# Kernel tuning notes

Hardware: AMD Instinct MI355X
Metric: run time of the kernel (lower is better)

The kernel has to match this reference:

```python
import jax, jax.numpy as jnp
import numpy as np

N, E = 50000, 800000
IN, HID, OUT, EH = 128, 64, 128, 32  # node dims, edge-MLP hidden=32
N_ETYPES, N_NTYPES = 3, 2


def setup_inputs() -> dict:
    key = jax.random.key(0)
    ks = jax.random.split(key, 12)
    w = lambda k, shape, fan: jax.random.normal(k, shape, jnp.float32) / np.float32(np.sqrt(fan))
    nf = jax.random.normal(ks[0], (N, IN), jnp.float32)
    edge_index = jax.random.randint(ks[1], (2, E), 0, N, dtype=jnp.int32)
    edge_type = jax.random.randint(ks[2], (E,), 0, N_ETYPES, dtype=jnp.int32)
    node_type = jax.random.randint(ks[3], (N,), 0, N_NTYPES, dtype=jnp.int32)
    return {
        "nf": nf,
        "edge_index": edge_index,
        "edge_type": edge_type,
        "node_type": node_type,
        # layer 0: 128 -> 64
        "eW0": w(ks[4], (N_ETYPES, 2 * IN, EH), 2 * IN),
        "eb0": jax.random.normal(ks[5], (N_ETYPES, EH), jnp.float32) * 0.01,
        "nW0": w(ks[6], (N_NTYPES, N_ETYPES * EH, HID), N_ETYPES * EH),
        "nb0": jax.random.normal(ks[7], (N_NTYPES, HID), jnp.float32) * 0.01,
        # layer 1: 64 -> 128
        "eW1": w(ks[8], (N_ETYPES, 2 * HID, EH), 2 * HID),
        "eb1": jax.random.normal(ks[9], (N_ETYPES, EH), jnp.float32) * 0.01,
        "nW1": w(ks[10], (N_NTYPES, N_ETYPES * EH, OUT), N_ETYPES * EH),
        "nb1": jax.random.normal(ks[11], (N_NTYPES, OUT), jnp.float32) * 0.01,
    }


def _layer(nf, eW, eb, nW, nb, src, dst, edge_type, node_type):
    """One GraphNeuralNetLayer: per-edge-type message MLP + mean-scatter, then per-node-type update MLP."""
    n = nf.shape[0]
    # edge gather + concat: [E, 2*in]
    feat = jnp.concatenate([nf[src], nf[dst]], axis=-1)
    msgs = []
    for e in range(eW.shape[0]):  # fixed, small number of edge types
        m = jax.nn.relu(feat @ eW[e] + eb[e])            # [E, EH]
        mask = (edge_type == e).astype(nf.dtype)          # select this edge type
        s = jax.ops.segment_sum(m * mask[:, None], dst, num_segments=n)
        cnt = jax.ops.segment_sum(mask, dst, num_segments=n)
        # mean over mailbox; nodes with no type-e in-edges get zeros
        msgs.append(s / jnp.maximum(cnt, 1.0)[:, None])
    h = jnp.concatenate(msgs, axis=-1)                    # [N, 3*EH]
    out0 = jax.nn.relu(h @ nW[0] + nb[0])
    out1 = jax.nn.relu(h @ nW[1] + nb[1])
    return jnp.where((node_type == 0)[:, None], out0, out1)


def reference(nf, edge_index, edge_type, node_type, eW0, eb0, nW0, nb0, eW1, eb1, nW1, nb1):
    src, dst = edge_index[0], edge_index[1]
    h = _layer(nf, eW0, eb0, nW0, nb0, src, dst, edge_type, node_type)   # [N, 64]
    return _layer(h, eW1, eb1, nW1, nb1, src, dst, edge_type, node_type) # [N, 128]
```

## Files before the change

kernel.cpp:

```cpp
#include <hip/hip_runtime.h>


typedef __attribute__((ext_vector_type(8))) short bf16x8_t;
typedef __attribute__((ext_vector_type(4))) float f32x4_t;
typedef _Float16 f16;
typedef __attribute__((ext_vector_type(4))) _Float16 f16x4_t;
typedef __attribute__((ext_vector_type(8))) _Float16 f16x8_t;

__device__ __forceinline__ void cvt_split(float x, unsigned short& h, unsigned short& l) {
  unsigned u = __float_as_uint(x);
  unsigned rh = u + 0x7FFFu + ((u >> 16) & 1u);
  h = (unsigned short)(rh >> 16);
  float xh = __uint_as_float((unsigned)h << 16);
  float xl = x - xh;
  unsigned v = __float_as_uint(xl);
  unsigned rl = v + 0x7FFFu + ((v >> 16) & 1u);
  l = (unsigned short)(rl >> 16);
}


template <int IN, int OUT>
__device__ __forceinline__ void prep_dev(int id,
                                         const float* __restrict__ eW,
                                         float* __restrict__ wfh,
                                         float* __restrict__ wfl,
                                         const float* __restrict__ nW,
                                         float* __restrict__ wnh,
                                         float* __restrict__ wnl) {
  constexpr int KC = IN / 32;
  constexpr int CT = OUT / 16;
  if (id < 12 * KC * 64) {
    int lane = id & 63;
    int fk = id >> 6;
    int kc = fk % KC, ct = fk / KC;
    int n = ct * 16 + (lane & 15);
    int kb = kc * 32 + ((lane >> 4) & 3) * 8;
    int half = (n >= 96) ? 1 : 0;
    int jj = n - 96 * half;
    int e = jj >> 5, o = jj & 31;
    const float* wp = eW + ((size_t)((e * 2 + half) * IN) + kb) * 32 + o;
    bf16x8_t hv, lv;
#pragma unroll
    for (int j = 0; j < 8; ++j) {
      unsigned short h, l;
      cvt_split(wp[(size_t)j * 32], h, l);
      hv[j] = (short)h;
      lv[j] = (short)l;
    }
    *(bf16x8_t*)(wfh + (size_t)id * 4) = hv;
    *(bf16x8_t*)(wfl + (size_t)id * 4) = lv;
    return;
  }
  int id2 = id - 12 * KC * 64;
  if (id2 >= 2 * CT * 3 * 64) return;
  int lane = id2 & 63;
  int fk = id2 >> 6;
  int kc = fk % 3;
  int ct = (fk / 3) % CT;
  int t = fk / (3 * CT);
  const float* wp = nW + ((size_t)t * 96 + kc * 32 + ((lane >> 4) & 3) * 8) * OUT +
                    ct * 16 + (lane & 15);
  bf16x8_t hv, lv;
#pragma unroll
  for (int j = 0; j < 8; ++j) {
    unsigned short h, l;
    cvt_split(wp[(size_t)j * OUT], h, l);
    hv[j] = (short)h;
    lv[j] = (short)l;
  }
  *(bf16x8_t*)(wnh + (size_t)id2 * 4) = hv;
  *(bf16x8_t*)(wnl + (size_t)id2 * 4) = lv;
}

__global__ __launch_bounds__(256) void prep_all(const float* __restrict__ eW0,
                                                float* __restrict__ wf0h, float* __restrict__ wf0l,
                                                const float* __restrict__ nW1,
                                                float* __restrict__ wn1h, float* __restrict__ wn1l,
                                                const float* __restrict__ eW1,
                                                float* __restrict__ wf1h, float* __restrict__ wf1l,
                                                const float* __restrict__ nW0,
                                                float* __restrict__ wn0h, float* __restrict__ wn0l,
                                                int* __restrict__ deg8, int zn4,
                                                int* __restrict__ tcnt) {
  int bid = blockIdx.x;
  if (bid < 24) {
    int id = bid * 256 + threadIdx.x;
    int4* zb = (int4*)deg8;
    for (int z = id; z < zn4; z += 24 * 256) zb[z] = make_int4(0, 0, 0, 0);
    if (id < 2) tcnt[id] = 0;
    prep_dev<128, 128>(id, eW0, wf0h, wf0l, nW1, wn1h, wn1l);
  } else {
    int id = (bid - 24) * 256 + threadIdx.x;
    prep_dev<64, 64>(id, eW1, wf1h, wf1l, nW0, wn0h, wn0l);
  }
}


template <int IN>
__device__ __forceinline__ void proj_dev(int bid,
                                         const float* __restrict__ X,
                                         const float* __restrict__ wfh,
                                         const float* __restrict__ wfl,
                                         f16* __restrict__ P, int n) {
  constexpr int KC = IN / 32;
  __shared__ short Ah[4 * KC * 64 * 8];
  __shared__ short Al[4 * KC * 64 * 8];
  const int tx = threadIdx.x;
  const int base = bid * 64;

  for (int q = tx; q < 4 * KC * 64; q += 256) {
    int lane = q & 63;
    int fk = q >> 6;
    int kc = fk % KC, nt = fk / KC;
    int node = base + nt * 16 + (lane & 15);
    int kb = kc * 32 + ((lane >> 4) & 3) * 8;
    float xs[8];
    if (node < n) {
      float4 a = *(const float4*)(X + (size_t)node * IN + kb);
      float4 b = *(const float4*)(X + (size_t)node * IN + kb + 4);
      xs[0] = a.x; xs[1] = a.y; xs[2] = a.z; xs[3] = a.w;
      xs[4] = b.x; xs[5] = b.y; xs[6] = b.z; xs[7] = b.w;
    } else {
#pragma unroll
      for (int j = 0; j < 8; ++j) xs[j] = 0.f;
    }
    bf16x8_t hv, lv;
#pragma unroll
    for (int j = 0; j < 8; ++j) {
      unsigned short h, l;
      cvt_split(xs[j], h, l);
      hv[j] = (short)h;
      lv[j] = (short)l;
    }
    *(bf16x8_t*)(Ah + (size_t)q * 8) = hv;
    *(bf16x8_t*)(Al + (size_t)q * 8) = lv;
  }
  __syncthreads();

  const int wave = tx >> 6;
  const int lane = tx & 63;

  f32x4_t acc[4][3];
#pragma unroll
  for (int nt = 0; nt < 4; ++nt)
#pragma unroll
    for (int c = 0; c < 3; ++c) acc[nt][c] = (f32x4_t){0.f, 0.f, 0.f, 0.f};

  for (int kc = 0; kc < KC; ++kc) {
    bf16x8_t Bh[3], Bl[3];
#pragma unroll
    for (int c = 0; c < 3; ++c) {
      int ct = wave * 3 + c;
      size_t idx = ((size_t)(ct * KC + kc) * 64 + lane) * 4;
      Bh[c] = *(const bf16x8_t*)(wfh + idx);
      Bl[c] = *(const bf16x8_t*)(wfl + idx);
    }
#pragma unroll
    for (int nt = 0; nt < 4; ++nt) {
      size_t idx = ((size_t)(nt * KC + kc) * 64 + lane) * 8;
      bf16x8_t ah = *(const bf16x8_t*)(Ah + idx);
      bf16x8_t al = *(const bf16x8_t*)(Al + idx);
#pragma unroll
      for (int c = 0; c < 3; ++c) {
        acc[nt][c] = __builtin_amdgcn_mfma_f32_16x16x32_bf16(ah, Bh[c], acc[nt][c], 0, 0, 0);
        acc[nt][c] = __builtin_amdgcn_mfma_f32_16x16x32_bf16(ah, Bl[c], acc[nt][c], 0, 0, 0);
        acc[nt][c] = __builtin_amdgcn_mfma_f32_16x16x32_bf16(al, Bh[c], acc[nt][c], 0, 0, 0);
      }
    }
  }

  const int row0 = ((lane >> 4) & 3) * 4;
  const int col = lane & 15;
#pragma unroll
  for (int nt = 0; nt < 4; ++nt) {
#pragma unroll
    for (int c = 0; c < 3; ++c) {
      int jcol = (wave * 3 + c) * 16 + col;
#pragma unroll
      for (int r = 0; r < 4; ++r) {
        int node = base + nt * 16 + row0 + r;
        if (node < n) P[(size_t)node * 192 + jcol] = (f16)acc[nt][c][r];
      }
    }
  }
}

template <int IN>
__global__ __launch_bounds__(256) void proj_mfma(const float* __restrict__ X,
                                                 const float* __restrict__ wfh,
                                                 const float* __restrict__ wfl,
                                                 f16* __restrict__ P, int n) {
  proj_dev<IN>(blockIdx.x, X, wfh, wfl, P, n);
}


__global__ __launch_bounds__(256) void fused_rpp(const float* __restrict__ X,
                                                 const float* __restrict__ wfh,
                                                 const float* __restrict__ wfl,
                                                 f16* __restrict__ P, int n, int pgrid,
                                                 const int* __restrict__ dst,
                                                 int* __restrict__ deg8,
                                                 int* __restrict__ rank, int E, int egrid,
                                                 const int* __restrict__ ntype,
                                                 int* __restrict__ idxbuf,
                                                 int* __restrict__ tcnt, int ncap) {
  int bid = blockIdx.x;
  int pb = bid / 5;
  if ((bid % 5) == 0 && pb < pgrid) {
    proj_dev<128>(pb, X, wfh, wfl, P, n);
    return;
  }
  int nproj_before = (bid % 5 == 0) ? pb : (pb + 1);
  if (nproj_before > pgrid) nproj_before = pgrid;
  int j = bid - nproj_before;
  if (j < egrid) {
    int i = j * 256 + threadIdx.x;
    if (i < E) {
      int d = dst[i];
      int r = (i >> 8) & 7;
      rank[i] = atomicAdd(&deg8[d * 8 + r], 1);
    }
    return;
  }
  j -= egrid;
  int i = j * 256 + threadIdx.x;
  int lane = threadIdx.x & 63;
  int t = (i < n) ? ntype[i] : -1;
  unsigned long long m0 = __ballot(t == 0);
  unsigned long long m1 = __ballot(t == 1);
  int b0 = 0, b1 = 0;
  if (lane == 0) {
    b0 = atomicAdd(&tcnt[0], (int)__popcll(m0));
    b1 = atomicAdd(&tcnt[1], (int)__popcll(m1));
  }
  b0 = __shfl(b0, 0);
  b1 = __shfl(b1, 0);
  unsigned long long below = (1ull << lane) - 1ull;
  if (t == 0) idxbuf[b0 + (int)__popcll(m0 & below)] = i;
  else if (t == 1) idxbuf[ncap + b1 + (int)__popcll(m1 & below)] = i;
}


__global__ __launch_bounds__(256) void scan1_kernel(int* __restrict__ deg8,
                                                    int* __restrict__ rowstart,
                                                    int* __restrict__ bsum, int n) {
  __shared__ int tmp[256];
  int t = threadIdx.x;
  int base = blockIdx.x * 1024 + t * 4;
  int vdeg[4];
#pragma unroll
  for (int q = 0; q < 4; ++q) {
    int v = base + q;
    int d = 0;
    if (v < n) {
      int4 a = *(int4*)(deg8 + (size_t)v * 8);
      int4 b = *(int4*)(deg8 + (size_t)v * 8 + 4);
      int p1 = a.x, p2 = p1 + a.y, p3 = p2 + a.z, p4 = p3 + a.w;
      int p5 = p4 + b.x, p6 = p5 + b.y, p7 = p6 + b.z;
      d = p7 + b.w;
      *(int4*)(deg8 + (size_t)v * 8) = make_int4(0, p1, p2, p3);
      *(int4*)(deg8 + (size_t)v * 8 + 4) = make_int4(p4, p5, p6, p7);
    }
    vdeg[q] = d;
  }
  int s = vdeg[0] + vdeg[1] + vdeg[2] + vdeg[3];
  tmp[t] = s;
  __syncthreads();
  for (int off = 1; off < 256; off <<= 1) {
    int u = (t >= off) ? tmp[t - off] : 0;
    __syncthreads();
    tmp[t] += u;
    __syncthreads();
  }
  int excl = tmp[t] - s;
  if (base < n)     rowstart[base]     = excl;
  if (base + 1 < n) rowstart[base + 1] = excl + vdeg[0];
  if (base + 2 < n) rowstart[base + 2] = excl + vdeg[0] + vdeg[1];
  if (base + 3 < n) rowstart[base + 3] = excl + vdeg[0] + vdeg[1] + vdeg[2];
  if (t == 255) bsum[blockIdx.x] = tmp[255];
}

__global__ __launch_bounds__(64) void scan2_kernel(const int* __restrict__ bsum,
                                                   int* __restrict__ boff, int nb,
                                                   int* __restrict__ rowstart, int n) {
  int lane = threadIdx.x;
  int v = (lane < nb) ? bsum[lane] : 0;
  int incl = v;
  for (int off = 1; off < 64; off <<= 1) {
    int u = __shfl_up(incl, off, 64);
    if (lane >= off) incl += u;
  }
  if (lane < nb) boff[lane] = incl - v;
  if (lane == 63) rowstart[n] = incl;
}

__global__ __launch_bounds__(256) void fill_kernel(const int* __restrict__ src,
                                                   const int* __restrict__ dst,
                                                   const int* __restrict__ etype,
                                                   const int* __restrict__ rank,
                                                   const int* __restrict__ rowstart,
                                                   const int* __restrict__ boff,
                                                   const int* __restrict__ deg8,
                                                   int* __restrict__ edata, int E) {
  int i = blockIdx.x * 256 + threadIdx.x;
  if (i < E) {
    int d = dst[i];
    int r = (i >> 8) & 7;
    int et = etype[i];
    int pos = rowstart[d] + boff[d >> 10] + deg8[d * 8 + r] + rank[i];
    edata[pos] = src[i] * 384 + et * 65;
  }
}


#define ACC_EDGEH(pk, v)                                              \
  {                                                                   \
    int et_ = (pk) & 3;                                               \
    bool e0_ = (et_ == 0), e1_ = (et_ == 1), e2_ = (et_ == 2);        \
    _Pragma("unroll")                                                 \
    for (int j = 0; j < 4; ++j) {                                     \
      float pb_ = e0_ ? pdb0[j] : (e1_ ? pdb1[j] : pdb2[j]);          \
      float m_ = fmaxf((float)(v)[j] + pb_, 0.f);                     \
      a0[j] += e0_ ? m_ : 0.f;                                        \
      a1[j] += e1_ ? m_ : 0.f;                                        \
      a2[j] += e2_ ? m_ : 0.f;                                        \
    }                                                                 \
    c0 += e0_; c1 += e1_;                                             \
  }

__global__ __launch_bounds__(256) void aggregate_kernel(const f16* __restrict__ P,
                                                        const int* __restrict__ rowstart,
                                                        const int* __restrict__ boff,
                                                        const int* __restrict__ edata,
                                                        const float* __restrict__ eb,
                                                        f16* __restrict__ h, int n) {
  int wid = (blockIdx.x * 256 + threadIdx.x) >> 6;
  if (wid >= n) return;
  int lane = threadIdx.x & 63;
  int co = (lane & 7) * 4;
  int cb = co * 2;
  int slot = lane >> 3;
  const f16* Pd = P + (size_t)wid * 192 + 96;
  float pdb0[4], pdb1[4], pdb2[4];
  {
    f16x4_t d0 = *(const f16x4_t*)(Pd + co);
    f16x4_t d1 = *(const f16x4_t*)(Pd + 32 + co);
    f16x4_t d2 = *(const f16x4_t*)(Pd + 64 + co);
    float4 e0 = *(const float4*)(eb + co);
    float4 e1 = *(const float4*)(eb + 32 + co);
    float4 e2 = *(const float4*)(eb + 64 + co);
    pdb0[0] = (float)d0[0] + e0.x; pdb0[1] = (float)d0[1] + e0.y;
    pdb0[2] = (float)d0[2] + e0.z; pdb0[3] = (float)d0[3] + e0.w;
    pdb1[0] = (float)d1[0] + e1.x; pdb1[1] = (float)d1[1] + e1.y;
    pdb1[2] = (float)d1[2] + e1.z; pdb1[3] = (float)d1[3] + e1.w;
    pdb2[0] = (float)d2[0] + e2.x; pdb2[1] = (float)d2[1] + e2.y;
    pdb2[2] = (float)d2[2] + e2.z; pdb2[3] = (float)d2[3] + e2.w;
  }
  int s = rowstart[wid] + boff[wid >> 10];
  int e = rowstart[wid + 1] + ((wid + 1 < n) ? boff[(wid + 1) >> 10] : 0);
  const char* Pb = (const char*)P;
  float a0[4], a1[4], a2[4];
#pragma unroll
  for (int j = 0; j < 4; ++j) { a0[j] = 0.f; a1[j] = 0.f; a2[j] = 0.f; }
  int c0 = 0, c1 = 0;
  for (int i = s + slot; i < e; i += 16) {
    int p0 = edata[i];
    int p1 = 3;
    int ii = i + 8;
    if (ii < e) p1 = edata[ii];
    f16x4_t v0 = *(const f16x4_t*)(Pb + (size_t)(p0 & ~3) + cb);
    f16x4_t v1 = *(const f16x4_t*)(Pb + (size_t)(p1 & ~3) + cb);
    ACC_EDGEH(p0, v0)
    ACC_EDGEH(p1, v1)
  }
#pragma unroll
  for (int off = 8; off < 64; off <<= 1) {
#pragma unroll
    for (int j = 0; j < 4; ++j) {
      a0[j] += __shfl_xor(a0[j], off);
      a1[j] += __shfl_xor(a1[j], off);
      a2[j] += __shfl_xor(a2[j], off);
    }
    c0 += __shfl_xor(c0, off);
    c1 += __shfl_xor(c1, off);
  }
  if (slot == 0) {
    int total = e - s;
    float d0 = fmaxf((float)c0, 1.f);
    float d1 = fmaxf((float)c1, 1.f);
    float d2 = fmaxf((float)(total - c0 - c1), 1.f);
    f16* hn = h + (size_t)wid * 96;
    f16x4_t o0, o1, o2;
#pragma unroll
    for (int j = 0; j < 4; ++j) {
      o0[j] = (f16)(a0[j] / d0);
      o1[j] = (f16)(a1[j] / d1);
      o2[j] = (f16)(a2[j] / d2);
    }
    *(f16x4_t*)(hn + co)      = o0;
    *(f16x4_t*)(hn + 32 + co) = o1;
    *(f16x4_t*)(hn + 64 + co) = o2;
  }
}


template <int OUT>
__global__ __launch_bounds__(256) void mlp2_mfma(const f16* __restrict__ H,
                                                 const float* __restrict__ wnh,
                                                 const float* __restrict__ wnl,
                                                 const float* __restrict__ nb,
                                                 const int* __restrict__ idxbuf,
                                                 const int* __restrict__ tcnt,
                                                 float* __restrict__ out, int ncap) {
  constexpr int CT = OUT / 16;
  constexpr int CW = CT / 4;
  __shared__ short Ah[12 * 64 * 8];
  __shared__ short Al[12 * 64 * 8];

  int c0 = tcnt[0];
  int nb0 = (c0 + 63) >> 6;
  int t, base, cnt;
  if ((int)blockIdx.x < nb0) {
    t = 0; base = blockIdx.x << 6; cnt = c0;
  } else {
    t = 1; base = ((int)blockIdx.x - nb0) << 6; cnt = tcnt[1];
    if (base >= cnt) return;
  }
  const int* il = idxbuf + (size_t)t * ncap;
  const float* bias = nb + t * OUT;

  const int tx = threadIdx.x;
  for (int q = tx; q < 12 * 64; q += 256) {
    int lane = q & 63;
    int fk = q >> 6;
    int kc = fk % 3, mt = fk / 3;
    int slot = base + mt * 16 + (lane & 15);
    int kb = kc * 32 + ((lane >> 4) & 3) * 8;
    float xs[8];
    if (slot < cnt) {
      int row = il[slot];
      f16x8_t a = *(const f16x8_t*)(H + (size_t)row * 96 + kb);
#pragma unroll
      for (int j = 0; j < 8; ++j) xs[j] = (float)a[j];
    } else {
#pragma unroll
      for (int j = 0; j < 8; ++j) xs[j] = 0.f;
    }
    bf16x8_t hv, lv;
#pragma unroll
    for (int j = 0; j < 8; ++j) {
      unsigned short h, l;
      cvt_split(xs[j], h, l);
      hv[j] = (short)h;
      lv[j] = (short)l;
    }
    *(bf16x8_t*)(Ah + (size_t)q * 8) = hv;
    *(bf16x8_t*)(Al + (size_t)q * 8) = lv;
  }
  __syncthreads();

  const int wave = tx >> 6;
  const int lane = tx & 63;

  f32x4_t acc[4][CW];
#pragma unroll
  for (int mt = 0; mt < 4; ++mt)
#pragma unroll
    for (int c = 0; c < CW; ++c) acc[mt][c] = (f32x4_t){0.f, 0.f, 0.f, 0.f};

  for (int kc = 0; kc < 3; ++kc) {
    bf16x8_t Bh[CW], Bl[CW];
#pragma unroll
    for (int c = 0; c < CW; ++c) {
      int ct = wave * CW + c;
      size_t idx = ((size_t)((t * CT + ct) * 3 + kc) * 64 + lane) * 4;
      Bh[c] = *(const bf16x8_t*)(wnh + idx);
      Bl[c] = *(const bf16x8_t*)(wnl + idx);
    }
#pragma unroll
    for (int mt = 0; mt < 4; ++mt) {
      size_t idx = ((size_t)((mt * 3 + kc) * 64) + lane) * 8;
      bf16x8_t ah = *(const bf16x8_t*)(Ah + idx);
      bf16x8_t al = *(const bf16x8_t*)(Al + idx);
#pragma unroll
      for (int c = 0; c < CW; ++c) {
        acc[mt][c] = __builtin_amdgcn_mfma_f32_16x16x32_bf16(ah, Bh[c], acc[mt][c], 0, 0, 0);
        acc[mt][c] = __builtin_amdgcn_mfma_f32_16x16x32_bf16(ah, Bl[c], acc[mt][c], 0, 0, 0);
        acc[mt][c] = __builtin_amdgcn_mfma_f32_16x16x32_bf16(al, Bh[c], acc[mt][c], 0, 0, 0);
      }
    }
  }

  const int row0 = ((lane >> 4) & 3) * 4;
  const int col = lane & 15;
#pragma unroll
  for (int mt = 0; mt < 4; ++mt) {
#pragma unroll
    for (int c = 0; c < CW; ++c) {
      int jcol = (wave * CW + c) * 16 + col;
      float bj = bias[jcol];
#pragma unroll
      for (int r = 0; r < 4; ++r) {
        int slot = base + mt * 16 + row0 + r;
        if (slot < cnt) {
          int row = il[slot];
          out[(size_t)row * OUT + jcol] = fmaxf(acc[mt][c][r] + bj, 0.f);
        }
      }
    }
  }
}


extern "C" void kernel_launch(void* const* d_in, const int* in_sizes, int n_in,
                              void* d_out, int out_size, void* d_ws, size_t ws_size,
                              hipStream_t stream) {
  const float* nf    = (const float*)d_in[0];
  const int*   eidx  = (const int*)d_in[1];
  const int*   etype = (const int*)d_in[2];
  const int*   ntype = (const int*)d_in[3];
  const float* eW0   = (const float*)d_in[4];
  const float* eb0   = (const float*)d_in[5];
  const float* nW0   = (const float*)d_in[6];
  const float* nb0   = (const float*)d_in[7];
  const float* eW1   = (const float*)d_in[8];
  const float* eb1   = (const float*)d_in[9];
  const float* nW1   = (const float*)d_in[10];
  const float* nb1   = (const float*)d_in[11];
  const int N = in_sizes[3];
  const int E = in_sizes[2];
  const int* srcv = eidx;
  const int* dstv = eidx + E;

  float* ws  = (float*)d_ws;
  f16*   P   = (f16*)ws;
  f16*   h96 = (f16*)(ws + (size_t)N * 192);
  float* h64 = ws + (size_t)N * 192 + (size_t)N * 96;
  int* rowstart = (int*)(h64 + (size_t)N * 64);
  int* tcnt     = rowstart + ((N + 4) & ~3);
  int* bsum     = tcnt + 2;
  int* boff     = bsum + 64;
  int* idxbuf   = boff + 64;
  int* edata    = idxbuf + 2 * N;
  float* wf0h   = (float*)(edata + E);
  float* wf0l   = wf0h + 12288;
  float* wf1h   = wf0l + 12288;
  float* wf1l   = wf1h + 6144;
  float* wn0h   = wf1l + 6144;
  float* wn0l   = wn0h + 6144;
  float* wn1h   = wn0l + 6144;
  float* wn1l   = wn1h + 12288;
  int* rank     = (int*)(ws + (size_t)N * 192);
  int* deg8     = (int*)h64;

  const int nsb = (N + 1023) / 1024;
  const int egrid = (E + 255) / 256;
  const int pargrid = (N + 255) / 256;
  const int pgrid = (N + 63) / 64;

  prep_all<<<36, 256, 0, stream>>>(eW0, wf0h, wf0l, nW1, wn1h, wn1l,
                                   eW1, wf1h, wf1l, nW0, wn0h, wn0l,
                                   deg8, N * 2, tcnt);
  fused_rpp<<<pgrid + egrid + pargrid, 256, 0, stream>>>(
      nf, wf0h, wf0l, P, N, pgrid,
      dstv, deg8, rank, E, egrid,
      ntype, idxbuf, tcnt, N);
  scan1_kernel<<<nsb, 256, 0, stream>>>(deg8, rowstart, bsum, N);
  scan2_kernel<<<1, 64, 0, stream>>>(bsum, boff, nsb, rowstart, N);
  fill_kernel<<<egrid, 256, 0, stream>>>(srcv, dstv, etype, rank, rowstart, boff, deg8, edata, E);

  int agrid = (N + 3) / 4;
  int mgrid = (N + 63) / 64 + 2;

  aggregate_kernel<<<agrid, 256, 0, stream>>>(P, rowstart, boff, edata, eb0, h96, N);
  mlp2_mfma<64><<<mgrid, 256, 0, stream>>>(h96, wn0h, wn0l, nb0, idxbuf, tcnt, h64, N);

  proj_mfma<64><<<pgrid, 256, 0, stream>>>(h64, wf1h, wf1l, P, N);
  aggregate_kernel<<<agrid, 256, 0, stream>>>(P, rowstart, boff, edata, eb1, h96, N);
  mlp2_mfma<128><<<mgrid, 256, 0, stream>>>(h96, wn1h, wn1l, nb1, idxbuf, tcnt, (float*)d_out, N);
}
```

Measured before the change: 278.8 us.

## Fuse layer-0 node MLP with layer-1 projection; single-pass scan with atomic block offsets

The layer-0 per-node-type MLP and the layer-1 edge projection now run in one kernel. The 64-wide hidden result is re-split into bf16 hi/lo in shared memory and multiplied straight into P, so the fp32 h64 intermediate is no longer written and read back and one launch is dropped. The two-kernel scan is replaced by one kernel that gets block offsets from an atomicAdd and writes absolute offsets into deg8, rowstart and a new rowend array. This simplifies the index math in fill and aggregate. The atomic block order makes the CSR edge order nondeterministic, which can change float summation order, and the fused kernel uses more registers.

```diff
diff --git a/kernel.cpp b/kernel.cpp
--- a/kernel.cpp
+++ b/kernel.cpp
@@ -81,13 +81,15 @@
                                                 const float* __restrict__ nW0,
                                                 float* __restrict__ wn0h, float* __restrict__ wn0l,
                                                 int* __restrict__ deg8, int zn4,
-                                                int* __restrict__ tcnt) {
+                                                int* __restrict__ tcnt,
+                                                int* __restrict__ gsum) {
   int bid = blockIdx.x;
   if (bid < 24) {
     int id = bid * 256 + threadIdx.x;
     int4* zb = (int4*)deg8;
     for (int z = id; z < zn4; z += 24 * 256) zb[z] = make_int4(0, 0, 0, 0);
     if (id < 2) tcnt[id] = 0;
+    if (id == 2) gsum[0] = 0;
     prep_dev<128, 128>(id, eW0, wf0h, wf0l, nW1, wn1h, wn1l);
   } else {
     int id = (bid - 24) * 256 + threadIdx.x;
@@ -183,14 +185,6 @@
       }
     }
   }
-}
-
-template <int IN>
-__global__ __launch_bounds__(256) void proj_mfma(const float* __restrict__ X,
-                                                 const float* __restrict__ wfh,
-                                                 const float* __restrict__ wfl,
-                                                 f16* __restrict__ P, int n) {
-  proj_dev<IN>(blockIdx.x, X, wfh, wfl, P, n);
 }
 
 
@@ -241,27 +235,31 @@
 }
 
 
-__global__ __launch_bounds__(256) void scan1_kernel(int* __restrict__ deg8,
-                                                    int* __restrict__ rowstart,
-                                                    int* __restrict__ bsum, int n) {
+__global__ __launch_bounds__(256) void scan_abs_kernel(int* __restrict__ deg8,
+                                                       int* __restrict__ rowstart,
+                                                       int* __restrict__ rowend,
+                                                       int* __restrict__ gsum, int n) {
   __shared__ int tmp[256];
+  __shared__ int bbs;
   int t = threadIdx.x;
   int base = blockIdx.x * 1024 + t * 4;
   int vdeg[4];
+  int4 pa[4], pb[4];
 #pragma unroll
   for (int q = 0; q < 4; ++q) {
     int v = base + q;
     int d = 0;
+    int4 a = make_int4(0, 0, 0, 0), b = make_int4(0, 0, 0, 0);
     if (v < n) {
-      int4 a = *(int4*)(deg8 + (size_t)v * 8);
-      int4 b = *(int4*)(deg8 + (size_t)v * 8 + 4);
+      a = *(int4*)(deg8 + (size_t)v * 8);
+      b = *(int4*)(deg8 + (size_t)v * 8 + 4);
       int p1 = a.x, p2 = p1 + a.y, p3 = p2 + a.z, p4 = p3 + a.w;
       int p5 = p4 + b.x, p6 = p5 + b.y, p7 = p6 + b.z;
       d = p7 + b.w;
-      *(int4*)(deg8 + (size_t)v * 8) = make_int4(0, p1, p2, p3);
-      *(int4*)(deg8 + (size_t)v * 8 + 4) = make_int4(p4, p5, p6, p7);
-    }
-    vdeg[q] = d;
+      a = make_int4(0, p1, p2, p3);
+      b = make_int4(p4, p5, p6, p7);
+    }
+    pa[q] = a; pb[q] = b; vdeg[q] = d;
   }
   int s = vdeg[0] + vdeg[1] + vdeg[2] + vdeg[3];
   tmp[t] = s;
@@ -273,33 +271,29 @@
     __syncthreads();
   }
   int excl = tmp[t] - s;
-  if (base < n)     rowstart[base]     = excl;
-  if (base + 1 < n) rowstart[base + 1] = excl + vdeg[0];
-  if (base + 2 < n) rowstart[base + 2] = excl + vdeg[0] + vdeg[1];
-  if (base + 3 < n) rowstart[base + 3] = excl + vdeg[0] + vdeg[1] + vdeg[2];
-  if (t == 255) bsum[blockIdx.x] = tmp[255];
-}
-
-__global__ __launch_bounds__(64) void scan2_kernel(const int* __restrict__ bsum,
-                                                   int* __restrict__ boff, int nb,
-                                                   int* __restrict__ rowstart, int n) {
-  int lane = threadIdx.x;
-  int v = (lane < nb) ? bsum[lane] : 0;
-  int incl = v;
-  for (int off = 1; off < 64; off <<= 1) {
-    int u = __shfl_up(incl, off, 64);
-    if (lane >= off) incl += u;
-  }
-  if (lane < nb) boff[lane] = incl - v;
-  if (lane == 63) rowstart[n] = incl;
+  if (t == 255) bbs = atomicAdd(gsum, tmp[255]);
+  __syncthreads();
+  int st = bbs + excl;
+#pragma unroll
+  for (int q = 0; q < 4; ++q) {
+    int v = base + q;
+    if (v < n) {
+      rowstart[v] = st;
+      rowend[v] = st + vdeg[q];
+      int4 a = pa[q], b = pb[q];
+      a.x += st; a.y += st; a.z += st; a.w += st;
+      b.x += st; b.y += st; b.z += st; b.w += st;
+      *(int4*)(deg8 + (size_t)v * 8) = a;
+      *(int4*)(deg8 + (size_t)v * 8 + 4) = b;
+    }
+    st += vdeg[q];
+  }
 }
 
 __global__ __launch_bounds__(256) void fill_kernel(const int* __restrict__ src,
                                                    const int* __restrict__ dst,
                                                    const int* __restrict__ etype,
                                                    const int* __restrict__ rank,
-                                                   const int* __restrict__ rowstart,
-                                                   const int* __restrict__ boff,
                                                    const int* __restrict__ deg8,
                                                    int* __restrict__ edata, int E) {
   int i = blockIdx.x * 256 + threadIdx.x;
@@ -307,7 +301,7 @@
     int d = dst[i];
     int r = (i >> 8) & 7;
     int et = etype[i];
-    int pos = rowstart[d] + boff[d >> 10] + deg8[d * 8 + r] + rank[i];
+    int pos = deg8[d * 8 + r] + rank[i];
     edata[pos] = src[i] * 384 + et * 65;
   }
 }
@@ -330,7 +324,7 @@
 
 __global__ __launch_bounds__(256) void aggregate_kernel(const f16* __restrict__ P,
                                                         const int* __restrict__ rowstart,
-                                                        const int* __restrict__ boff,
+                                                        const int* __restrict__ rowend,
                                                         const int* __restrict__ edata,
                                                         const float* __restrict__ eb,
                                                         f16* __restrict__ h, int n) {
@@ -356,8 +350,8 @@
     pdb2[0] = (float)d2[0] + e2.x; pdb2[1] = (float)d2[1] + e2.y;
     pdb2[2] = (float)d2[2] + e2.z; pdb2[3] = (float)d2[3] + e2.w;
   }
-  int s = rowstart[wid] + boff[wid >> 10];
-  int e = rowstart[wid + 1] + ((wid + 1 < n) ? boff[(wid + 1) >> 10] : 0);
+  int s = rowstart[wid];
+  int e = rowend[wid];
   const char* Pb = (const char*)P;
   float a0[4], a1[4], a2[4];
 #pragma unroll
@@ -400,6 +394,158 @@
     *(f16x4_t*)(hn + co)      = o0;
     *(f16x4_t*)(hn + 32 + co) = o1;
     *(f16x4_t*)(hn + 64 + co) = o2;
+  }
+}
+
+
+__global__ __launch_bounds__(256) void mlp2proj64(const f16* __restrict__ H,
+                                                  const float* __restrict__ wnh,
+                                                  const float* __restrict__ wnl,
+                                                  const float* __restrict__ nb,
+                                                  const int* __restrict__ idxbuf,
+                                                  const int* __restrict__ tcnt,
+                                                  const float* __restrict__ wfh,
+                                                  const float* __restrict__ wfl,
+                                                  f16* __restrict__ P, int ncap) {
+  __shared__ short Ah[12 * 64 * 8];
+  __shared__ short Al[12 * 64 * 8];
+
+  int c0n = tcnt[0];
+  int nb0 = (c0n + 63) >> 6;
+  int t, base, cnt;
+  if ((int)blockIdx.x < nb0) {
+    t = 0; base = blockIdx.x << 6; cnt = c0n;
+  } else {
+    t = 1; base = ((int)blockIdx.x - nb0) << 6; cnt = tcnt[1];
+    if (base >= cnt) return;
+  }
+  const int* il = idxbuf + (size_t)t * ncap;
+  const float* bias = nb + t * 64;
+
+  const int tx = threadIdx.x;
+  for (int q = tx; q < 12 * 64; q += 256) {
+    int lane = q & 63;
+    int fk = q >> 6;
+    int kc = fk % 3, mt = fk / 3;
+    int slot = base + mt * 16 + (lane & 15);
+    int kb = kc * 32 + ((lane >> 4) & 3) * 8;
+    float xs[8];
+    if (slot < cnt) {
+      int row = il[slot];
+      f16x8_t a = *(const f16x8_t*)(H + (size_t)row * 96 + kb);
+#pragma unroll
+      for (int j = 0; j < 8; ++j) xs[j] = (float)a[j];
+    } else {
+#pragma unroll
+      for (int j = 0; j < 8; ++j) xs[j] = 0.f;
+    }
+    bf16x8_t hv, lv;
+#pragma unroll
+    for (int j = 0; j < 8; ++j) {
+      unsigned short h, l;
+      cvt_split(xs[j], h, l);
+      hv[j] = (short)h;
+      lv[j] = (short)l;
+    }
+    *(bf16x8_t*)(Ah + (size_t)q * 8) = hv;
+    *(bf16x8_t*)(Al + (size_t)q * 8) = lv;
+  }
+  __syncthreads();
+
+  const int wave = tx >> 6;
+  const int lane = tx & 63;
+  const int col = lane & 15;
+
+  f32x4_t acc[4];
+#pragma unroll
+  for (int mt = 0; mt < 4; ++mt) acc[mt] = (f32x4_t){0.f, 0.f, 0.f, 0.f};
+
+  for (int kc = 0; kc < 3; ++kc) {
+    bf16x8_t Bh, Bl;
+    {
+      size_t idx = ((size_t)((t * 4 + wave) * 3 + kc) * 64 + lane) * 4;
+      Bh = *(const bf16x8_t*)(wnh + idx);
+      Bl = *(const bf16x8_t*)(wnl + idx);
+    }
+#pragma unroll
+    for (int mt = 0; mt < 4; ++mt) {
+      size_t idx = ((size_t)((mt * 3 + kc) * 64) + lane) * 8;
+      bf16x8_t ah = *(const bf16x8_t*)(Ah + idx);
+      bf16x8_t al = *(const bf16x8_t*)(Al + idx);
+      acc[mt] = __builtin_amdgcn_mfma_f32_16x16x32_bf16(ah, Bh, acc[mt], 0, 0, 0);
+      acc[mt] = __builtin_amdgcn_mfma_f32_16x16x32_bf16(ah, Bl, acc[mt], 0, 0, 0);
+      acc[mt] = __builtin_amdgcn_mfma_f32_16x16x32_bf16(al, Bh, acc[mt], 0, 0, 0);
+    }
+  }
+  __syncthreads();
+
+  {
+    float bj = bias[wave * 16 + col];
+    int kcp = wave >> 1;
+    int kq = (wave * 2 + (col >> 3)) & 3;
+    int jj = col & 7;
+#pragma unroll
+    for (int mt = 0; mt < 4; ++mt) {
+#pragma unroll
+      for (int r = 0; r < 4; ++r) {
+        int srel = mt * 16 + ((lane >> 4) & 3) * 4 + r;
+        float v = 0.f;
+        if (base + srel < cnt) v = fmaxf(acc[mt][r] + bj, 0.f);
+        unsigned short h, l;
+        cvt_split(v, h, l);
+        int lane2 = (srel & 15) + (kq << 4);
+        int q = (mt * 2 + kcp) * 64 + lane2;
+        Ah[(size_t)q * 8 + jj] = (short)h;
+        Al[(size_t)q * 8 + jj] = (short)l;
+      }
+    }
+  }
+  __syncthreads();
+
+  f32x4_t pacc[4][3];
+#pragma unroll
+  for (int nt = 0; nt < 4; ++nt)
+#pragma unroll
+    for (int c = 0; c < 3; ++c) pacc[nt][c] = (f32x4_t){0.f, 0.f, 0.f, 0.f};
+
+  for (int kc = 0; kc < 2; ++kc) {
+    bf16x8_t Bh[3], Bl[3];
+#pragma unroll
+    for (int c = 0; c < 3; ++c) {
+      int ct = wave * 3 + c;
+      size_t idx = ((size_t)(ct * 2 + kc) * 64 + lane) * 4;
+      Bh[c] = *(const bf16x8_t*)(wfh + idx);
+      Bl[c] = *(const bf16x8_t*)(wfl + idx);
+    }
+#pragma unroll
+    for (int nt = 0; nt < 4; ++nt) {
+      size_t idx = ((size_t)((nt * 2 + kc) * 64) + lane) * 8;
+      bf16x8_t ah = *(const bf16x8_t*)(Ah + idx);
+      bf16x8_t al = *(const bf16x8_t*)(Al + idx);
+#pragma unroll
+      for (int c = 0; c < 3; ++c) {
+        pacc[nt][c] = __builtin_amdgcn_mfma_f32_16x16x32_bf16(ah, Bh[c], pacc[nt][c], 0, 0, 0);
+        pacc[nt][c] = __builtin_amdgcn_mfma_f32_16x16x32_bf16(ah, Bl[c], pacc[nt][c], 0, 0, 0);
+        pacc[nt][c] = __builtin_amdgcn_mfma_f32_16x16x32_bf16(al, Bh[c], pacc[nt][c], 0, 0, 0);
+      }
+    }
+  }
+
+  const int row0 = ((lane >> 4) & 3) * 4;
+#pragma unroll
+  for (int nt = 0; nt < 4; ++nt) {
+#pragma unroll
+    for (int c = 0; c < 3; ++c) {
+      int jcol = (wave * 3 + c) * 16 + col;
+#pragma unroll
+      for (int r = 0; r < 4; ++r) {
+        int slot = base + nt * 16 + row0 + r;
+        if (slot < cnt) {
+          int row = il[slot];
+          P[(size_t)row * 192 + jcol] = (f16)pacc[nt][c][r];
+        }
+      }
+    }
   }
 }
 
@@ -535,8 +681,8 @@
   float* ws  = (float*)d_ws;
   f16*   P   = (f16*)ws;
   f16*   h96 = (f16*)(ws + (size_t)N * 192);
-  float* h64 = ws + (size_t)N * 192 + (size_t)N * 96;
-  int* rowstart = (int*)(h64 + (size_t)N * 64);
+  float* h64r = ws + (size_t)N * 192 + (size_t)N * 96;
+  int* rowstart = (int*)(h64r + (size_t)N * 64);
   int* tcnt     = rowstart + ((N + 4) & ~3);
   int* bsum     = tcnt + 2;
   int* boff     = bsum + 64;
@@ -551,7 +697,9 @@
   float* wn1h   = wn0l + 6144;
   float* wn1l   = wn1h + 12288;
   int* rank     = (int*)(ws + (size_t)N * 192);
-  int* deg8     = (int*)h64;
+  int* deg8     = (int*)h64r;
+  int* rowend   = deg8 + (size_t)8 * N;
+  int* gsum     = bsum;
 
   const int nsb = (N + 1023) / 1024;
   const int egrid = (E + 255) / 256;
@@ -560,22 +708,20 @@
 
   prep_all<<<36, 256, 0, stream>>>(eW0, wf0h, wf0l, nW1, wn1h, wn1l,
                                    eW1, wf1h, wf1l, nW0, wn0h, wn0l,
-                                   deg8, N * 2, tcnt);
+                                   deg8, N * 2, tcnt, gsum);
   fused_rpp<<<pgrid + egrid + pargrid, 256, 0, stream>>>(
       nf, wf0h, wf0l, P, N, pgrid,
       dstv, deg8, rank, E, egrid,
       ntype, idxbuf, tcnt, N);
-  scan1_kernel<<<nsb, 256, 0, stream>>>(deg8, rowstart, bsum, N);
-  scan2_kernel<<<1, 64, 0, stream>>>(bsum, boff, nsb, rowstart, N);
-  fill_kernel<<<egrid, 256, 0, stream>>>(srcv, dstv, etype, rank, rowstart, boff, deg8, edata, E);
+  scan_abs_kernel<<<nsb, 256, 0, stream>>>(deg8, rowstart, rowend, gsum, N);
+  fill_kernel<<<egrid, 256, 0, stream>>>(srcv, dstv, etype, rank, deg8, edata, E);
 
   int agrid = (N + 3) / 4;
   int mgrid = (N + 63) / 64 + 2;
 
-  aggregate_kernel<<<agrid, 256, 0, stream>>>(P, rowstart, boff, edata, eb0, h96, N);
-  mlp2_mfma<64><<<mgrid, 256, 0, stream>>>(h96, wn0h, wn0l, nb0, idxbuf, tcnt, h64, N);
-
-  proj_mfma<64><<<pgrid, 256, 0, stream>>>(h64, wf1h, wf1l, P, N);
-  aggregate_kernel<<<agrid, 256, 0, stream>>>(P, rowstart, boff, edata, eb1, h96, N);
+  aggregate_kernel<<<agrid, 256, 0, stream>>>(P, rowstart, rowend, edata, eb0, h96, N);
+  mlp2proj64<<<mgrid, 256, 0, stream>>>(h96, wn0h, wn0l, nb0, idxbuf, tcnt,
+                                        wf1h, wf1l, P, N);
+  aggregate_kernel<<<agrid, 256, 0, stream>>>(P, rowstart, rowend, edata, eb1, h96, N);
   mlp2_mfma<128><<<mgrid, 256, 0, stream>>>(h96, wn1h, wn1l, nb1, idxbuf, tcnt, (float*)d_out, N);
 }
```

Measured after the change: 282.9 us. Within noise of the previous version (+1.5%).

## Merge scan passes via atomic block offsets and split projection across fused kernels

Applied to the files above, without the earlier changes.

Replaces the two-pass scan (scan1 plus scan2) with a single kernel that takes each block's base offset from a global atomic counter and writes absolute row starts, row ends and per-slot offsets. The fill kernel and the aggregation then drop the boff lookups. The layer-0 projection is split in half, with one half interleaved into the degree-count kernel and the other into the fill kernel, to hide launch gaps and balance work. The atomic block ordering yields a valid but nondeterministic CSR layout, which is fine because aggregation only needs each node's own [start, end) range.

```diff
diff --git a/kernel.cpp b/kernel.cpp
--- a/kernel.cpp
+++ b/kernel.cpp
@@ -81,13 +81,15 @@
                                                 const float* __restrict__ nW0,
                                                 float* __restrict__ wn0h, float* __restrict__ wn0l,
                                                 int* __restrict__ deg8, int zn4,
-                                                int* __restrict__ tcnt) {
+                                                int* __restrict__ tcnt,
+                                                int* __restrict__ gsum) {
   int bid = blockIdx.x;
   if (bid < 24) {
     int id = bid * 256 + threadIdx.x;
     int4* zb = (int4*)deg8;
     for (int z = id; z < zn4; z += 24 * 256) zb[z] = make_int4(0, 0, 0, 0);
     if (id < 2) tcnt[id] = 0;
+    if (id == 2) gsum[0] = 0;
     prep_dev<128, 128>(id, eW0, wf0h, wf0l, nW1, wn1h, wn1l);
   } else {
     int id = (bid - 24) * 256 + threadIdx.x;
@@ -194,24 +196,25 @@
 }
 
 
-__global__ __launch_bounds__(256) void fused_rpp(const float* __restrict__ X,
-                                                 const float* __restrict__ wfh,
-                                                 const float* __restrict__ wfl,
-                                                 f16* __restrict__ P, int n, int pgrid,
-                                                 const int* __restrict__ dst,
-                                                 int* __restrict__ deg8,
-                                                 int* __restrict__ rank, int E, int egrid,
-                                                 const int* __restrict__ ntype,
-                                                 int* __restrict__ idxbuf,
-                                                 int* __restrict__ tcnt, int ncap) {
+__global__ __launch_bounds__(256) void fusedA(const float* __restrict__ X,
+                                              const float* __restrict__ wfh,
+                                              const float* __restrict__ wfl,
+                                              f16* __restrict__ P, int n,
+                                              int npb, int pbase,
+                                              const int* __restrict__ dst,
+                                              int* __restrict__ deg8,
+                                              int* __restrict__ rank, int E, int egrid,
+                                              const int* __restrict__ ntype,
+                                              int* __restrict__ idxbuf,
+                                              int* __restrict__ tcnt, int ncap) {
   int bid = blockIdx.x;
-  int pb = bid / 5;
-  if ((bid % 5) == 0 && pb < pgrid) {
-    proj_dev<128>(pb, X, wfh, wfl, P, n);
+  int pb = bid / 9;
+  if ((bid % 9) == 0 && pb < npb) {
+    proj_dev<128>(pbase + pb, X, wfh, wfl, P, n);
     return;
   }
-  int nproj_before = (bid % 5 == 0) ? pb : (pb + 1);
-  if (nproj_before > pgrid) nproj_before = pgrid;
+  int nproj_before = (bid % 9 == 0) ? pb : (pb + 1);
+  if (nproj_before > npb) nproj_before = npb;
   int j = bid - nproj_before;
   if (j < egrid) {
     int i = j * 256 + threadIdx.x;
@@ -241,27 +244,31 @@
 }
 
 
-__global__ __launch_bounds__(256) void scan1_kernel(int* __restrict__ deg8,
-                                                    int* __restrict__ rowstart,
-                                                    int* __restrict__ bsum, int n) {
+__global__ __launch_bounds__(256) void scan_abs_kernel(int* __restrict__ deg8,
+                                                       int* __restrict__ rowstart,
+                                                       int* __restrict__ rowend,
+                                                       int* __restrict__ gsum, int n) {
   __shared__ int tmp[256];
+  __shared__ int bbs;
   int t = threadIdx.x;
   int base = blockIdx.x * 1024 + t * 4;
   int vdeg[4];
+  int4 pa[4], pb[4];
 #pragma unroll
   for (int q = 0; q < 4; ++q) {
     int v = base + q;
     int d = 0;
+    int4 a = make_int4(0, 0, 0, 0), b = make_int4(0, 0, 0, 0);
     if (v < n) {
-      int4 a = *(int4*)(deg8 + (size_t)v * 8);
-      int4 b = *(int4*)(deg8 + (size_t)v * 8 + 4);
+      a = *(int4*)(deg8 + (size_t)v * 8);
+      b = *(int4*)(deg8 + (size_t)v * 8 + 4);
       int p1 = a.x, p2 = p1 + a.y, p3 = p2 + a.z, p4 = p3 + a.w;
       int p5 = p4 + b.x, p6 = p5 + b.y, p7 = p6 + b.z;
       d = p7 + b.w;
-      *(int4*)(deg8 + (size_t)v * 8) = make_int4(0, p1, p2, p3);
-      *(int4*)(deg8 + (size_t)v * 8 + 4) = make_int4(p4, p5, p6, p7);
-    }
-    vdeg[q] = d;
+      a = make_int4(0, p1, p2, p3);
+      b = make_int4(p4, p5, p6, p7);
+    }
+    pa[q] = a; pb[q] = b; vdeg[q] = d;
   }
   int s = vdeg[0] + vdeg[1] + vdeg[2] + vdeg[3];
   tmp[t] = s;
@@ -273,41 +280,52 @@
     __syncthreads();
   }
   int excl = tmp[t] - s;
-  if (base < n)     rowstart[base]     = excl;
-  if (base + 1 < n) rowstart[base + 1] = excl + vdeg[0];
-  if (base + 2 < n) rowstart[base + 2] = excl + vdeg[0] + vdeg[1];
-  if (base + 3 < n) rowstart[base + 3] = excl + vdeg[0] + vdeg[1] + vdeg[2];
-  if (t == 255) bsum[blockIdx.x] = tmp[255];
-}
-
-__global__ __launch_bounds__(64) void scan2_kernel(const int* __restrict__ bsum,
-                                                   int* __restrict__ boff, int nb,
-                                                   int* __restrict__ rowstart, int n) {
-  int lane = threadIdx.x;
-  int v = (lane < nb) ? bsum[lane] : 0;
-  int incl = v;
-  for (int off = 1; off < 64; off <<= 1) {
-    int u = __shfl_up(incl, off, 64);
-    if (lane >= off) incl += u;
-  }
-  if (lane < nb) boff[lane] = incl - v;
-  if (lane == 63) rowstart[n] = incl;
-}
-
-__global__ __launch_bounds__(256) void fill_kernel(const int* __restrict__ src,
-                                                   const int* __restrict__ dst,
-                                                   const int* __restrict__ etype,
-                                                   const int* __restrict__ rank,
-                                                   const int* __restrict__ rowstart,
-                                                   const int* __restrict__ boff,
-                                                   const int* __restrict__ deg8,
-                                                   int* __restrict__ edata, int E) {
-  int i = blockIdx.x * 256 + threadIdx.x;
+  if (t == 255) bbs = atomicAdd(gsum, tmp[255]);
+  __syncthreads();
+  int st = bbs + excl;
+#pragma unroll
+  for (int q = 0; q < 4; ++q) {
+    int v = base + q;
+    if (v < n) {
+      rowstart[v] = st;
+      rowend[v] = st + vdeg[q];
+      int4 a = pa[q], b = pb[q];
+      a.x += st; a.y += st; a.z += st; a.w += st;
+      b.x += st; b.y += st; b.z += st; b.w += st;
+      *(int4*)(deg8 + (size_t)v * 8) = a;
+      *(int4*)(deg8 + (size_t)v * 8 + 4) = b;
+    }
+    st += vdeg[q];
+  }
+}
+
+
+__global__ __launch_bounds__(256) void fusedB(const float* __restrict__ X,
+                                              const float* __restrict__ wfh,
+                                              const float* __restrict__ wfl,
+                                              f16* __restrict__ P, int n,
+                                              int npb, int pbase,
+                                              const int* __restrict__ src,
+                                              const int* __restrict__ dst,
+                                              const int* __restrict__ etype,
+                                              const int* __restrict__ rank,
+                                              const int* __restrict__ deg8,
+                                              int* __restrict__ edata, int E) {
+  int bid = blockIdx.x;
+  int pb = bid / 9;
+  if ((bid % 9) == 0 && pb < npb) {
+    proj_dev<128>(pbase + pb, X, wfh, wfl, P, n);
+    return;
+  }
+  int nproj_before = (bid % 9 == 0) ? pb : (pb + 1);
+  if (nproj_before > npb) nproj_before = npb;
+  int j = bid - nproj_before;
+  int i = j * 256 + threadIdx.x;
   if (i < E) {
     int d = dst[i];
     int r = (i >> 8) & 7;
     int et = etype[i];
-    int pos = rowstart[d] + boff[d >> 10] + deg8[d * 8 + r] + rank[i];
+    int pos = deg8[d * 8 + r] + rank[i];
     edata[pos] = src[i] * 384 + et * 65;
   }
 }
@@ -330,7 +348,7 @@
 
 __global__ __launch_bounds__(256) void aggregate_kernel(const f16* __restrict__ P,
                                                         const int* __restrict__ rowstart,
-                                                        const int* __restrict__ boff,
+                                                        const int* __restrict__ rowend,
                                                         const int* __restrict__ edata,
                                                         const float* __restrict__ eb,
                                                         f16* __restrict__ h, int n) {
@@ -356,8 +374,8 @@
     pdb2[0] = (float)d2[0] + e2.x; pdb2[1] = (float)d2[1] + e2.y;
     pdb2[2] = (float)d2[2] + e2.z; pdb2[3] = (float)d2[3] + e2.w;
   }
-  int s = rowstart[wid] + boff[wid >> 10];
-  int e = rowstart[wid + 1] + ((wid + 1 < n) ? boff[(wid + 1) >> 10] : 0);
+  int s = rowstart[wid];
+  int e = rowend[wid];
   const char* Pb = (const char*)P;
   float a0[4], a1[4], a2[4];
 #pragma unroll
@@ -537,10 +555,10 @@
   f16*   h96 = (f16*)(ws + (size_t)N * 192);
   float* h64 = ws + (size_t)N * 192 + (size_t)N * 96;
   int* rowstart = (int*)(h64 + (size_t)N * 64);
-  int* tcnt     = rowstart + ((N + 4) & ~3);
-  int* bsum     = tcnt + 2;
-  int* boff     = bsum + 64;
-  int* idxbuf   = boff + 64;
+  int* rowend   = rowstart + N;
+  int* tcnt     = rowend + N;
+  int* gsum     = tcnt + 2;
+  int* idxbuf   = gsum + 2;
   int* edata    = idxbuf + 2 * N;
   float* wf0h   = (float*)(edata + E);
   float* wf0l   = wf0h + 12288;
@@ -557,25 +575,27 @@
   const int egrid = (E + 255) / 256;
   const int pargrid = (N + 255) / 256;
   const int pgrid = (N + 63) / 64;
+  const int npbA = (pgrid + 1) / 2;
+  const int npbB = pgrid - npbA;
 
   prep_all<<<36, 256, 0, stream>>>(eW0, wf0h, wf0l, nW1, wn1h, wn1l,
                                    eW1, wf1h, wf1l, nW0, wn0h, wn0l,
-                                   deg8, N * 2, tcnt);
-  fused_rpp<<<pgrid + egrid + pargrid, 256, 0, stream>>>(
-      nf, wf0h, wf0l, P, N, pgrid,
+                                   deg8, N * 2, tcnt, gsum);
+  fusedA<<<npbA + egrid + pargrid, 256, 0, stream>>>(
+      nf, wf0h, wf0l, P, N, npbA, 0,
       dstv, deg8, rank, E, egrid,
       ntype, idxbuf, tcnt, N);
-  scan1_kernel<<<nsb, 256, 0, stream>>>(deg8, rowstart, bsum, N);
-  scan2_kernel<<<1, 64, 0, stream>>>(bsum, boff, nsb, rowstart, N);
-  fill_kernel<<<egrid, 256, 0, stream>>>(srcv, dstv, etype, rank, rowstart, boff, deg8, edata, E);
+  scan_abs_kernel<<<nsb, 256, 0, stream>>>(deg8, rowstart, rowend, gsum, N);
+  fusedB<<<npbB + egrid, 256, 0, stream>>>(
+      nf, wf0h, wf0l, P, N, npbB, npbA,
+      srcv, dstv, etype, rank, deg8, edata, E);
 
   int agrid = (N + 3) / 4;
   int mgrid = (N + 63) / 64 + 2;
 
-  aggregate_kernel<<<agrid, 256, 0, stream>>>(P, rowstart, boff, edata, eb0, h96, N);
+  aggregate_kernel<<<agrid, 256, 0, stream>>>(P, rowstart, rowend, edata, eb0, h96, N);
   mlp2_mfma<64><<<mgrid, 256, 0, stream>>>(h96, wn0h, wn0l, nb0, idxbuf, tcnt, h64, N);
-
   proj_mfma<64><<<pgrid, 256, 0, stream>>>(h64, wf1h, wf1l, P, N);
-  aggregate_kernel<<<agrid, 256, 0, stream>>>(P, rowstart, boff, edata, eb1, h96, N);
+  aggregate_kernel<<<agrid, 256, 0, stream>>>(P, rowstart, rowend, edata, eb1, h96, N);
   mlp2_mfma<128><<<mgrid, 256, 0, stream>>>(h96, wn1h, wn1l, nb1, idxbuf, tcnt, (float*)d_out, N);
 }
```

New measurement: 280.4 us. Within noise of the previous version (+0.6%).
